# Optimization experiments

Hardware: AMD Instinct MI355X
Metric: run time of the kernel (lower is better)

## Reference

```python
import math
import jax, jax.numpy as jnp
import numpy as np

B, T, C, H = 4, 1024, 1024, 16
HD = C // H
BLOCK = 1024


def setup_inputs() -> dict:
    key = jax.random.key(0)
    k0, k1, k2, k3 = jax.random.split(key, 4)
    x = jax.random.normal(k0, (B, T, C), dtype=jnp.float32)
    # torch Linear weight is (out, in); we store (in, out) and apply x @ W + b
    W_attn = jax.random.normal(k1, (C, 3 * C), dtype=jnp.float32) * 0.02
    b_attn = jnp.zeros((3 * C,), dtype=jnp.float32)
    W_proj = jax.random.normal(k2, (C, C), dtype=jnp.float32) * 0.02
    b_proj = jnp.zeros((C,), dtype=jnp.float32)
    # rel_pos_emb: (n_head, block_size, head_dim), std 0.02 (leading 1 dim dropped)
    rel_pos_emb = jax.random.normal(k3, (H, BLOCK, HD), dtype=jnp.float32) * 0.02
    return {"x": x, "W_attn": W_attn, "b_attn": b_attn,
            "W_proj": W_proj, "b_proj": b_proj, "rel_pos_emb": rel_pos_emb}


def reference(x, W_attn, b_attn, W_proj, b_proj, rel_pos_emb):
    Bx, Tx, Cx = x.shape
    qkv = x @ W_attn + b_attn                      # (B, T, 3C)
    q, k, v = jnp.split(qkv, 3, axis=2)
    q = q.reshape(Bx, Tx, H, HD).transpose(0, 2, 1, 3)   # (B, H, T, hd)
    k = k.reshape(Bx, Tx, H, HD).transpose(0, 2, 1, 3)
    v = v.reshape(Bx, Tx, H, HD).transpose(0, 2, 1, 3)

    att = jnp.einsum('bhid,bhjd->bhij', q, k)      # (B, H, T, T)

    # relative position score: pos[b,h,i,j] = sum_d E[h, clamp(i-j,0), d] * k[b,h,j,d]
    # compute P[b,h,r,j] = <E[h,r,:], k[b,h,j,:]> then gather r = clamp(i-j, 0)
    rng = jnp.arange(Tx)
    dist = jnp.clip(rng[:, None] - rng[None, :], 0, None)          # (T, T)
    P = jnp.einsum('hrd,bhjd->bhrj', rel_pos_emb[:, :Tx], k)       # (B, H, T, T)
    pos_score = jnp.take_along_axis(P, dist[None, None, :, :], axis=2)
    att = att + pos_score

    att = att * (1.0 / math.sqrt(HD))
    causal = jnp.tril(jnp.ones((Tx, Tx), dtype=bool))
    att = jnp.where(causal[None, None], att, -jnp.inf)
    att = jax.nn.softmax(att, axis=-1)
    # dropout p=0.0 -> identity
    y = jnp.einsum('bhij,bhjd->bhid', att, v)      # (B, H, T, hd)
    y = y.transpose(0, 2, 1, 3).reshape(Bx, Tx, Cx)
    return y @ W_proj + b_proj
```

## Files before the change

kernel.cpp:

```cpp
#include <hip/hip_runtime.h>


typedef __bf16 bf16x8 __attribute__((ext_vector_type(8)));
typedef float f32x4 __attribute__((ext_vector_type(4)));
typedef unsigned short ushort_t;

#define T_SEQ 1024
#define NHEAD 16
#define HDIM 64
#define PLANE 4194304

__device__ __forceinline__ float bf2f(ushort_t h) {
    unsigned int u = ((unsigned int)h) << 16;
    float f; __builtin_memcpy(&f, &u, 4); return f;
}
__device__ __forceinline__ ushort_t f2bf(float f) {
    unsigned int u; __builtin_memcpy(&u, &f, 4);
    u = u + 0x7FFFu + ((u >> 16) & 1u);
    return (ushort_t)(u >> 16);
}

__global__ __launch_bounds__(256) void sentinel_kernel(float* out, int n, float val) {
    const int i = blockIdx.x * 256 + threadIdx.x;
    if (i < n) out[i] = val;
}

__global__ __launch_bounds__(256) void convert_bf16(
    const float* __restrict__ src, ushort_t* __restrict__ dst, int n)
{
    const int i = (blockIdx.x * 256 + threadIdx.x) * 4;
    if (i < n) {
        const float4 v = *reinterpret_cast<const float4*>(src + i);
        union { unsigned long long u; ushort_t s[4]; } o;
        o.s[0] = f2bf(v.x); o.s[1] = f2bf(v.y); o.s[2] = f2bf(v.z); o.s[3] = f2bf(v.w);
        *reinterpret_cast<unsigned long long*>(dst + i) = o.u;
    }
}

__global__ __launch_bounds__(256) void transpose_bf16(
    const float* __restrict__ W, ushort_t* __restrict__ Wt, int Kdim, int Ndim)
{
    __shared__ ushort_t t[64][65];
    const int n0 = blockIdx.x * 64, k0 = blockIdx.y * 64;
    const int cx = threadIdx.x & 63, ry = threadIdx.x >> 6;
#pragma unroll
    for (int i = 0; i < 16; i++) {
        const int r = ry + i * 4;
        t[r][cx] = f2bf(W[(size_t)(k0 + r) * Ndim + n0 + cx]);
    }
    __syncthreads();
#pragma unroll
    for (int i = 0; i < 16; i++) {
        const int r = ry + i * 4;
        Wt[(size_t)(n0 + r) * Kdim + k0 + cx] = t[cx][r];
    }
}

template <int MODE>
__global__ __launch_bounds__(256) void gemm128(
    const ushort_t* __restrict__ A16, const ushort_t* __restrict__ Bt,
    const float* __restrict__ bias, void* __restrict__ out_,
    int Ndim, int Kdim)
{
    __shared__ __align__(16) ushort_t As[128 * 32];
    __shared__ __align__(16) ushort_t Bs[128 * 32];

    const int tid = threadIdx.x;
    const int w = tid >> 6;
    const int lane = tid & 63;
    const int l15 = lane & 15;
    const int quad = lane >> 4;
    const int m0 = blockIdx.y * 128, n0 = blockIdx.x * 128;
    const int wm = (w & 1) * 64, wn = (w >> 1) * 64;

    f32x4 acc[4][4];
#pragma unroll
    for (int mt = 0; mt < 4; mt++)
#pragma unroll
        for (int nt = 0; nt < 4; nt++) acc[mt][nt] = (f32x4){0.f, 0.f, 0.f, 0.f};

    for (int kk = 0; kk < Kdim; kk += 32) {
        __syncthreads();
#pragma unroll
        for (int t = 0; t < 2; t++) {
            const int chunk = w * 128 + t * 64 + lane;
            const int row = chunk >> 2, kc = (chunk & 3) * 8;
            __builtin_amdgcn_global_load_lds(
                (const __attribute__((address_space(1))) void*)
                    (A16 + (size_t)(m0 + row) * Kdim + kk + kc),
                (__attribute__((address_space(3))) void*)
                    (As + (size_t)(w * 128 + t * 64) * 8), 16, 0, 0);
            __builtin_amdgcn_global_load_lds(
                (const __attribute__((address_space(1))) void*)
                    (Bt + (size_t)(n0 + row) * Kdim + kk + kc),
                (__attribute__((address_space(3))) void*)
                    (Bs + (size_t)(w * 128 + t * 64) * 8), 16, 0, 0);
        }
        __syncthreads();

        bf16x8 af[4], bf[4];
#pragma unroll
        for (int mt = 0; mt < 4; mt++)
            af[mt] = *reinterpret_cast<const bf16x8*>(&As[(wm + mt * 16 + l15) * 32 + quad * 8]);
#pragma unroll
        for (int nt = 0; nt < 4; nt++)
            bf[nt] = *reinterpret_cast<const bf16x8*>(&Bs[(wn + nt * 16 + l15) * 32 + quad * 8]);
#pragma unroll
        for (int mt = 0; mt < 4; mt++)
#pragma unroll
            for (int nt = 0; nt < 4; nt++)
                acc[mt][nt] = __builtin_amdgcn_mfma_f32_16x16x32_bf16(
                    af[mt], bf[nt], acc[mt][nt], 0, 0, 0);
    }

#pragma unroll
    for (int mt = 0; mt < 4; mt++)
#pragma unroll
        for (int nt = 0; nt < 4; nt++) {
            const int n = n0 + wn + nt * 16 + l15;
            const float bv = bias[n];
#pragma unroll
            for (int r = 0; r < 4; r++) {
                const int m = m0 + wm + mt * 16 + quad * 4 + r;
                const float val = acc[mt][nt][r] + bv;
                if (MODE == 0) {
                    ushort_t* ws = (ushort_t*)out_;
                    const int which = n >> 10;
                    const int cc = n & 1023;
                    const int h = cc >> 6, d = cc & 63;
                    const int b = m >> 10, t = m & 1023;
                    const int bh = b * NHEAD + h;
                    if (which == 2)
                        ws[(size_t)2 * PLANE + (size_t)bh * 65536 + (size_t)d * 1024 + t] = f2bf(val);
                    else
                        ws[(size_t)which * PLANE + ((size_t)bh * T_SEQ + t) * HDIM + d] = f2bf(val);
                } else {
                    ((float*)out_)[(size_t)m * Ndim + n] = val;
                }
            }
        }
}

__global__ __launch_bounds__(256) void flash_attn(
    const ushort_t* __restrict__ qp, const ushort_t* __restrict__ kp,
    const ushort_t* __restrict__ vTp, const ushort_t* __restrict__ E16,
    ushort_t* __restrict__ y16)
{
    __shared__ __align__(16) ushort_t Qs[64 * 72];
    __shared__ __align__(16) ushort_t Ks[64 * 72];
    __shared__ __align__(16) ushort_t Vt[64 * 72];
    __shared__ __align__(16) ushort_t Es[128 * 72];
    __shared__ __align__(16) ushort_t Ps[128 * 72];

    const int bh = blockIdx.y;
    const int h = bh & (NHEAD - 1);
    const int b = bh >> 4;
    const int tid = threadIdx.x;
    const int w = tid >> 6;
    const int lane = tid & 63;
    const int l15 = lane & 15;
    const int quad = lane >> 4;

    const size_t base = (size_t)bh * T_SEQ * HDIM;
    const ushort_t* Eh = E16 + (size_t)h * T_SEQ * HDIM;
    const ushort_t* vTb = vTp + (size_t)bh * 65536;
    const float c1 = 0.125f * 1.44269504f;

    const int rq = tid >> 2, cq = (tid & 3) * 16;
    const int re = tid >> 1, ce = (tid & 1) * 32;

#pragma unroll 1
    for (int ph = 0; ph < 2; ph++) {
        const int it = ph ? (int)blockIdx.x : 15 - (int)blockIdx.x;
        const int i0 = it * 64;

        {
            const ushort_t* src = qp + base + (size_t)(i0 + rq) * HDIM + cq;
            *reinterpret_cast<uint4*>(&Qs[rq * 72 + cq]) = *reinterpret_cast<const uint4*>(src);
            *reinterpret_cast<uint4*>(&Qs[rq * 72 + cq + 8]) = *reinterpret_cast<const uint4*>(src + 8);
        }

        f32x4 o[4];
#pragma unroll
        for (int dt = 0; dt < 4; dt++) o[dt] = (f32x4){0.f, 0.f, 0.f, 0.f};
        float mrow[4], lrow[4];
#pragma unroll
        for (int r = 0; r < 4; r++) { mrow[r] = -3e38f; lrow[r] = 0.f; }

        for (int j0 = 0; j0 <= i0; j0 += 64) {
            const int d0 = i0 - j0;
            __syncthreads();
            {
                const ushort_t* ksrc = kp + base + (size_t)(j0 + rq) * HDIM + cq;
                *reinterpret_cast<uint4*>(&Ks[rq * 72 + cq]) = *reinterpret_cast<const uint4*>(ksrc);
                *reinterpret_cast<uint4*>(&Ks[rq * 72 + cq + 8]) = *reinterpret_cast<const uint4*>(ksrc + 8);
                const ushort_t* vsrc = vTb + (size_t)rq * 1024 + j0 + cq;
                *reinterpret_cast<uint4*>(&Vt[rq * 72 + cq]) = *reinterpret_cast<const uint4*>(vsrc);
                *reinterpret_cast<uint4*>(&Vt[rq * 72 + cq + 8]) = *reinterpret_cast<const uint4*>(vsrc + 8);
            }
            {
                int g = d0 - 64 + re;
                g = g < 0 ? 0 : (g > 1023 ? 1023 : g);
                const ushort_t* esrc = Eh + (size_t)g * HDIM + ce;
#pragma unroll
                for (int q16 = 0; q16 < 4; q16++)
                    *reinterpret_cast<uint4*>(&Es[re * 72 + ce + q16 * 8]) =
                        *reinterpret_cast<const uint4*>(esrc + q16 * 8);
            }
            __syncthreads();

            f32x4 s[4], pb[2][4];
#pragma unroll
            for (int nt = 0; nt < 4; nt++) {
                s[nt] = (f32x4){0.f, 0.f, 0.f, 0.f};
                pb[0][nt] = (f32x4){0.f, 0.f, 0.f, 0.f};
                pb[1][nt] = (f32x4){0.f, 0.f, 0.f, 0.f};
            }
#pragma unroll
            for (int ks = 0; ks < 2; ks++) {
                const int ko = ks * 32 + quad * 8;
                const bf16x8 aq  = *reinterpret_cast<const bf16x8*>(&Qs[(w * 16 + l15) * 72 + ko]);
                const bf16x8 ae0 = *reinterpret_cast<const bf16x8*>(&Es[(w * 32 + l15) * 72 + ko]);
                const bf16x8 ae1 = *reinterpret_cast<const bf16x8*>(&Es[(w * 32 + 16 + l15) * 72 + ko]);
#pragma unroll
                for (int nt = 0; nt < 4; nt++) {
                    const bf16x8 bk = *reinterpret_cast<const bf16x8*>(&Ks[(nt * 16 + l15) * 72 + ko]);
                    s[nt] = __builtin_amdgcn_mfma_f32_16x16x32_bf16(aq, bk, s[nt], 0, 0, 0);
                    pb[0][nt] = __builtin_amdgcn_mfma_f32_16x16x32_bf16(ae0, bk, pb[0][nt], 0, 0, 0);
                    pb[1][nt] = __builtin_amdgcn_mfma_f32_16x16x32_bf16(ae1, bk, pb[1][nt], 0, 0, 0);
                }
            }
#pragma unroll
            for (int mf = 0; mf < 2; mf++)
#pragma unroll
                for (int nt = 0; nt < 4; nt++)
#pragma unroll
                    for (int r = 0; r < 4; r++)
                        Ps[(w * 32 + mf * 16 + quad * 4 + r) * 72 + nt * 16 + l15] =
                            f2bf(pb[mf][nt][r]);
            __syncthreads();

            float pv[4][4], mnew[4];
#pragma unroll
            for (int r = 0; r < 4; r++) mnew[r] = mrow[r];
            const int brmin = 64 - d0;
#pragma unroll
            for (int nt = 0; nt < 4; nt++) {
                const int jl = nt * 16 + l15;
#pragma unroll
                for (int r = 0; r < 4; r++) {
                    const int il = w * 16 + quad * 4 + r;
                    float sv;
                    if (d0 == 0 && jl > il) {
                        sv = -3e38f;
                    } else {
                        int br = il - jl + 64;
                        br = br < brmin ? brmin : br;
                        sv = (s[nt][r] + bf2f(Ps[br * 72 + jl])) * c1;
                    }
                    pv[nt][r] = sv;
                    mnew[r] = fmaxf(mnew[r], sv);
                }
            }
#pragma unroll
            for (int r = 0; r < 4; r++)
#pragma unroll
                for (int off = 1; off < 16; off <<= 1)
                    mnew[r] = fmaxf(mnew[r], __shfl_xor(mnew[r], off, 64));
            float rowsum[4], alpha[4];
#pragma unroll
            for (int r = 0; r < 4; r++) { alpha[r] = exp2f(mrow[r] - mnew[r]); rowsum[r] = 0.f; }
#pragma unroll
            for (int nt = 0; nt < 4; nt++)
#pragma unroll
                for (int r = 0; r < 4; r++) {
                    const float p = exp2f(pv[nt][r] - mnew[r]);
                    pv[nt][r] = p;
                    rowsum[r] += p;
                }
#pragma unroll
            for (int r = 0; r < 4; r++) {
#pragma unroll
                for (int off = 1; off < 16; off <<= 1)
                    rowsum[r] += __shfl_xor(rowsum[r], off, 64);
                lrow[r] = lrow[r] * alpha[r] + rowsum[r];
                mrow[r] = mnew[r];
            }
#pragma unroll
            for (int dt = 0; dt < 4; dt++)
#pragma unroll
                for (int r = 0; r < 4; r++) o[dt][r] *= alpha[r];
#pragma unroll
            for (int nt = 0; nt < 4; nt++)
#pragma unroll
                for (int r = 0; r < 4; r++)
                    Es[(w * 16 + quad * 4 + r) * 72 + nt * 16 + l15] = f2bf(pv[nt][r]);
            __syncthreads();

#pragma unroll
            for (int ks = 0; ks < 2; ks++) {
                const int ko = ks * 32 + quad * 8;
                const bf16x8 ap = *reinterpret_cast<const bf16x8*>(&Es[(w * 16 + l15) * 72 + ko]);
#pragma unroll
                for (int dt = 0; dt < 4; dt++) {
                    const bf16x8 bv = *reinterpret_cast<const bf16x8*>(&Vt[(dt * 16 + l15) * 72 + ko]);
                    o[dt] = __builtin_amdgcn_mfma_f32_16x16x32_bf16(ap, bv, o[dt], 0, 0, 0);
                }
            }
        }

        float inv[4];
#pragma unroll
        for (int r = 0; r < 4; r++) inv[r] = 1.0f / lrow[r];
#pragma unroll
        for (int dt = 0; dt < 4; dt++)
#pragma unroll
            for (int r = 0; r < 4; r++) {
                const int il = w * 16 + quad * 4 + r;
                const int d = dt * 16 + l15;
                y16[((size_t)(b * T_SEQ + i0 + il)) * 1024 + h * 64 + d] = f2bf(o[dt][r] * inv[r]);
            }
    }
}

extern "C" void kernel_launch(void* const* d_in, const int* in_sizes, int n_in,
                              void* d_out, int out_size, void* d_ws, size_t ws_size,
                              hipStream_t stream) {
    float* out = (float*)d_out;

    const void* x = nullptr; const void* Wa = nullptr; const void* ba = nullptr;
    const void* Wp = nullptr; const void* bp = nullptr; const void* E = nullptr;
    int anomaly = 0;
    if (n_in != 6) {
        anomaly = 2;
    } else {
        int c1M = 0;
        for (int i = 0; i < 6; i++) {
            const int s = in_sizes[i];
            if      (s == 4194304) x  = d_in[i];
            else if (s == 3145728) Wa = d_in[i];
            else if (s == 3072)    ba = d_in[i];
            else if (s == 1024)    bp = d_in[i];
            else if (s == 1048576) { if (c1M == 0) Wp = d_in[i]; else E = d_in[i]; c1M++; }
            else anomaly = 1;
        }
        if (!x || !Wa || !ba || !Wp || !bp || !E || c1M != 2) anomaly = 1;
    }
    if (!anomaly && out_size != 4194304) anomaly = 3;
    if (!anomaly && ws_size < (size_t)52428800) anomaly = 4;
    if (anomaly) {
        sentinel_kernel<<<(out_size + 255) / 256, 256, 0, stream>>>(out, out_size, 1000.0f * anomaly);
        return;
    }

    ushort_t* ws  = (ushort_t*)d_ws;
    ushort_t* qp  = ws;
    ushort_t* kp  = ws + (size_t)PLANE;
    ushort_t* vTp = ws + (size_t)2 * PLANE;
    ushort_t* y16 = ws + (size_t)3 * PLANE;
    ushort_t* x16 = ws + (size_t)4 * PLANE;
    ushort_t* WaT = ws + (size_t)5 * PLANE;
    ushort_t* WpT = WaT + (size_t)3145728;
    ushort_t* E16 = WpT + (size_t)1048576;

    convert_bf16<<<4096, 256, 0, stream>>>((const float*)x, x16, 4194304);
    transpose_bf16<<<dim3(48, 16), 256, 0, stream>>>((const float*)Wa, WaT, 1024, 3072);
    transpose_bf16<<<dim3(16, 16), 256, 0, stream>>>((const float*)Wp, WpT, 1024, 1024);
    convert_bf16<<<1024, 256, 0, stream>>>((const float*)E, E16, 1048576);

    gemm128<0><<<dim3(24, 32), 256, 0, stream>>>(x16, WaT, (const float*)ba, (void*)ws, 3072, 1024);

    flash_attn<<<dim3(8, 64), 256, 0, stream>>>(qp, kp, vTp, E16, y16);

    gemm128<1><<<dim3(8, 32), 256, 0, stream>>>(y16, WpT, (const float*)bp, (void*)out, 1024, 1024);
}
```

Baseline: 238.3 us.

## Restructure attention: register Q, pre-shifted rel-pos scatter, MFMA row sums, separate V transpose

Several changes at once. The x and E conversions become a single launch. The QKV GEMM now writes V row-major into a temporary plane, and a new transpose kernel builds V^T, replacing the strided scattered stores. The attention kernel loads Q fragments straight into registers, scatters the relative-position scores into a shifted 64x64 tile so the softmax reads them with direct indexing, splits the masked diagonal tile into its own path, and gets the softmax denominator from an extra MFMA against a ones vector instead of shuffle reductions. The cost is one extra kernel launch and the V round trip through memory, plus a row sum computed from bf16-rounded probabilities.

New measurement: 222.3 us. 6.7% less time.

```diff
diff --git a/kernel.cpp b/kernel.cpp
--- a/kernel.cpp
+++ b/kernel.cpp
@@ -25,16 +25,19 @@
     if (i < n) out[i] = val;
 }
 
-__global__ __launch_bounds__(256) void convert_bf16(
-    const float* __restrict__ src, ushort_t* __restrict__ dst, int n)
+__global__ __launch_bounds__(256) void convert2(
+    const float* __restrict__ x, ushort_t* __restrict__ x16,
+    const float* __restrict__ E, ushort_t* __restrict__ E16)
 {
-    const int i = (blockIdx.x * 256 + threadIdx.x) * 4;
-    if (i < n) {
-        const float4 v = *reinterpret_cast<const float4*>(src + i);
-        union { unsigned long long u; ushort_t s[4]; } o;
-        o.s[0] = f2bf(v.x); o.s[1] = f2bf(v.y); o.s[2] = f2bf(v.z); o.s[3] = f2bf(v.w);
-        *reinterpret_cast<unsigned long long*>(dst + i) = o.u;
-    }
+    const int bid = blockIdx.x;
+    const float* src; ushort_t* dst; int base;
+    if (bid < 4096) { src = x; dst = x16; base = bid * 1024; }
+    else            { src = E; dst = E16; base = (bid - 4096) * 1024; }
+    const int i = base + (int)threadIdx.x * 4;
+    const float4 v = *reinterpret_cast<const float4*>(src + i);
+    union { unsigned long long u; ushort_t s[4]; } o;
+    o.s[0] = f2bf(v.x); o.s[1] = f2bf(v.y); o.s[2] = f2bf(v.z); o.s[3] = f2bf(v.w);
+    *reinterpret_cast<unsigned long long*>(dst + i) = o.u;
 }
 
 __global__ __launch_bounds__(256) void transpose_bf16(
@@ -53,6 +56,28 @@
     for (int i = 0; i < 16; i++) {
         const int r = ry + i * 4;
         Wt[(size_t)(n0 + r) * Kdim + k0 + cx] = t[cx][r];
+    }
+}
+
+__global__ __launch_bounds__(256) void transpose_v(
+    const ushort_t* __restrict__ v, ushort_t* __restrict__ vT)
+{
+    __shared__ ushort_t t[64][65];
+    const int bh = blockIdx.y;
+    const int t0 = blockIdx.x * 64;
+    const int cx = threadIdx.x & 63, ry = threadIdx.x >> 6;
+    const ushort_t* src = v + (size_t)bh * 65536;
+    ushort_t* dst = vT + (size_t)bh * 65536;
+#pragma unroll
+    for (int i = 0; i < 16; i++) {
+        const int r = ry + i * 4;
+        t[r][cx] = src[(size_t)(t0 + r) * HDIM + cx];
+    }
+    __syncthreads();
+#pragma unroll
+    for (int i = 0; i < 16; i++) {
+        const int d = ry + i * 4;
+        dst[(size_t)d * T_SEQ + t0 + cx] = t[cx][d];
     }
 }
 
@@ -126,14 +151,11 @@
                 if (MODE == 0) {
                     ushort_t* ws = (ushort_t*)out_;
                     const int which = n >> 10;
+                    const size_t pl = (which == 2) ? 3 : which;
                     const int cc = n & 1023;
                     const int h = cc >> 6, d = cc & 63;
                     const int b = m >> 10, t = m & 1023;
-                    const int bh = b * NHEAD + h;
-                    if (which == 2)
-                        ws[(size_t)2 * PLANE + (size_t)bh * 65536 + (size_t)d * 1024 + t] = f2bf(val);
-                    else
-                        ws[(size_t)which * PLANE + ((size_t)bh * T_SEQ + t) * HDIM + d] = f2bf(val);
+                    ws[pl * PLANE + ((size_t)(b * NHEAD + h) * T_SEQ + t) * HDIM + d] = f2bf(val);
                 } else {
                     ((float*)out_)[(size_t)m * Ndim + n] = val;
                 }
@@ -146,11 +168,10 @@
     const ushort_t* __restrict__ vTp, const ushort_t* __restrict__ E16,
     ushort_t* __restrict__ y16)
 {
-    __shared__ __align__(16) ushort_t Qs[64 * 72];
     __shared__ __align__(16) ushort_t Ks[64 * 72];
     __shared__ __align__(16) ushort_t Vt[64 * 72];
     __shared__ __align__(16) ushort_t Es[128 * 72];
-    __shared__ __align__(16) ushort_t Ps[128 * 72];
+    __shared__ __align__(16) ushort_t Ps[64 * 64 + 16];
 
     const int bh = blockIdx.y;
     const int h = bh & (NHEAD - 1);
@@ -169,23 +190,29 @@
     const int rq = tid >> 2, cq = (tid & 3) * 16;
     const int re = tid >> 1, ce = (tid & 1) * 32;
 
+    bf16x8 ones;
+#pragma unroll
+    for (int i = 0; i < 8; i++) ones[i] = (__bf16)1.0f;
+
 #pragma unroll 1
     for (int ph = 0; ph < 2; ph++) {
         const int it = ph ? (int)blockIdx.x : 15 - (int)blockIdx.x;
         const int i0 = it * 64;
 
+        bf16x8 qf[2];
         {
-            const ushort_t* src = qp + base + (size_t)(i0 + rq) * HDIM + cq;
-            *reinterpret_cast<uint4*>(&Qs[rq * 72 + cq]) = *reinterpret_cast<const uint4*>(src);
-            *reinterpret_cast<uint4*>(&Qs[rq * 72 + cq + 8]) = *reinterpret_cast<const uint4*>(src + 8);
+            const ushort_t* qrow = qp + base + (size_t)(i0 + w * 16 + l15) * HDIM;
+            qf[0] = *reinterpret_cast<const bf16x8*>(qrow + quad * 8);
+            qf[1] = *reinterpret_cast<const bf16x8*>(qrow + 32 + quad * 8);
         }
 
-        f32x4 o[4];
+        f32x4 o[4], o5;
 #pragma unroll
         for (int dt = 0; dt < 4; dt++) o[dt] = (f32x4){0.f, 0.f, 0.f, 0.f};
-        float mrow[4], lrow[4];
-#pragma unroll
-        for (int r = 0; r < 4; r++) { mrow[r] = -3e38f; lrow[r] = 0.f; }
+        o5 = (f32x4){0.f, 0.f, 0.f, 0.f};
+        float mrow[4];
+#pragma unroll
+        for (int r = 0; r < 4; r++) mrow[r] = -3e38f;
 
         for (int j0 = 0; j0 <= i0; j0 += 64) {
             const int d0 = i0 - j0;
@@ -194,7 +221,7 @@
                 const ushort_t* ksrc = kp + base + (size_t)(j0 + rq) * HDIM + cq;
                 *reinterpret_cast<uint4*>(&Ks[rq * 72 + cq]) = *reinterpret_cast<const uint4*>(ksrc);
                 *reinterpret_cast<uint4*>(&Ks[rq * 72 + cq + 8]) = *reinterpret_cast<const uint4*>(ksrc + 8);
-                const ushort_t* vsrc = vTb + (size_t)rq * 1024 + j0 + cq;
+                const ushort_t* vsrc = vTb + (size_t)rq * T_SEQ + j0 + cq;
                 *reinterpret_cast<uint4*>(&Vt[rq * 72 + cq]) = *reinterpret_cast<const uint4*>(vsrc);
                 *reinterpret_cast<uint4*>(&Vt[rq * 72 + cq + 8]) = *reinterpret_cast<const uint4*>(vsrc + 8);
             }
@@ -219,13 +246,12 @@
 #pragma unroll
             for (int ks = 0; ks < 2; ks++) {
                 const int ko = ks * 32 + quad * 8;
-                const bf16x8 aq  = *reinterpret_cast<const bf16x8*>(&Qs[(w * 16 + l15) * 72 + ko]);
                 const bf16x8 ae0 = *reinterpret_cast<const bf16x8*>(&Es[(w * 32 + l15) * 72 + ko]);
                 const bf16x8 ae1 = *reinterpret_cast<const bf16x8*>(&Es[(w * 32 + 16 + l15) * 72 + ko]);
 #pragma unroll
                 for (int nt = 0; nt < 4; nt++) {
                     const bf16x8 bk = *reinterpret_cast<const bf16x8*>(&Ks[(nt * 16 + l15) * 72 + ko]);
-                    s[nt] = __builtin_amdgcn_mfma_f32_16x16x32_bf16(aq, bk, s[nt], 0, 0, 0);
+                    s[nt] = __builtin_amdgcn_mfma_f32_16x16x32_bf16(qf[ks], bk, s[nt], 0, 0, 0);
                     pb[0][nt] = __builtin_amdgcn_mfma_f32_16x16x32_bf16(ae0, bk, pb[0][nt], 0, 0, 0);
                     pb[1][nt] = __builtin_amdgcn_mfma_f32_16x16x32_bf16(ae1, bk, pb[1][nt], 0, 0, 0);
                 }
@@ -233,33 +259,45 @@
 #pragma unroll
             for (int mf = 0; mf < 2; mf++)
 #pragma unroll
-                for (int nt = 0; nt < 4; nt++)
-#pragma unroll
-                    for (int r = 0; r < 4; r++)
-                        Ps[(w * 32 + mf * 16 + quad * 4 + r) * 72 + nt * 16 + l15] =
-                            f2bf(pb[mf][nt][r]);
+                for (int nt = 0; nt < 4; nt++) {
+                    const int jl = nt * 16 + l15;
+#pragma unroll
+                    for (int r = 0; r < 4; r++) {
+                        const int br = w * 32 + mf * 16 + quad * 4 + r;
+                        const int il_t = br - 64 + jl;
+                        const int addr = ((unsigned)il_t < 64u) ? il_t * 64 + jl : 4096;
+                        Ps[addr] = f2bf(pb[mf][nt][r]);
+                    }
+                }
             __syncthreads();
 
             float pv[4][4], mnew[4];
 #pragma unroll
             for (int r = 0; r < 4; r++) mnew[r] = mrow[r];
-            const int brmin = 64 - d0;
-#pragma unroll
-            for (int nt = 0; nt < 4; nt++) {
-                const int jl = nt * 16 + l15;
-#pragma unroll
-                for (int r = 0; r < 4; r++) {
-                    const int il = w * 16 + quad * 4 + r;
-                    float sv;
-                    if (d0 == 0 && jl > il) {
-                        sv = -3e38f;
-                    } else {
-                        int br = il - jl + 64;
-                        br = br < brmin ? brmin : br;
-                        sv = (s[nt][r] + bf2f(Ps[br * 72 + jl])) * c1;
+            const int il0 = w * 16 + quad * 4;
+            if (j0 < i0) {
+#pragma unroll
+                for (int nt = 0; nt < 4; nt++) {
+                    const int jl = nt * 16 + l15;
+#pragma unroll
+                    for (int r = 0; r < 4; r++) {
+                        const float sv = (s[nt][r] + bf2f(Ps[(il0 + r) * 64 + jl])) * c1;
+                        pv[nt][r] = sv;
+                        mnew[r] = fmaxf(mnew[r], sv);
                     }
-                    pv[nt][r] = sv;
-                    mnew[r] = fmaxf(mnew[r], sv);
+                }
+            } else {
+#pragma unroll
+                for (int nt = 0; nt < 4; nt++) {
+                    const int jl = nt * 16 + l15;
+#pragma unroll
+                    for (int r = 0; r < 4; r++) {
+                        const int il = il0 + r;
+                        float sv = (s[nt][r] + bf2f(Ps[il * 64 + jl])) * c1;
+                        if (jl > il) sv = -3e38f;
+                        pv[nt][r] = sv;
+                        mnew[r] = fmaxf(mnew[r], sv);
+                    }
                 }
             }
 #pragma unroll
@@ -267,29 +305,23 @@
 #pragma unroll
                 for (int off = 1; off < 16; off <<= 1)
                     mnew[r] = fmaxf(mnew[r], __shfl_xor(mnew[r], off, 64));
-            float rowsum[4], alpha[4];
-#pragma unroll
-            for (int r = 0; r < 4; r++) { alpha[r] = exp2f(mrow[r] - mnew[r]); rowsum[r] = 0.f; }
+            float alpha[4];
+#pragma unroll
+            for (int r = 0; r < 4; r++) {
+                alpha[r] = exp2f(mrow[r] - mnew[r]);
+                mrow[r] = mnew[r];
+            }
 #pragma unroll
             for (int nt = 0; nt < 4; nt++)
 #pragma unroll
-                for (int r = 0; r < 4; r++) {
-                    const float p = exp2f(pv[nt][r] - mnew[r]);
-                    pv[nt][r] = p;
-                    rowsum[r] += p;
-                }
-#pragma unroll
-            for (int r = 0; r < 4; r++) {
-#pragma unroll
-                for (int off = 1; off < 16; off <<= 1)
-                    rowsum[r] += __shfl_xor(rowsum[r], off, 64);
-                lrow[r] = lrow[r] * alpha[r] + rowsum[r];
-                mrow[r] = mnew[r];
-            }
+                for (int r = 0; r < 4; r++)
+                    pv[nt][r] = exp2f(pv[nt][r] - mnew[r]);
 #pragma unroll
             for (int dt = 0; dt < 4; dt++)
 #pragma unroll
                 for (int r = 0; r < 4; r++) o[dt][r] *= alpha[r];
+#pragma unroll
+            for (int r = 0; r < 4; r++) o5[r] *= alpha[r];
 #pragma unroll
             for (int nt = 0; nt < 4; nt++)
 #pragma unroll
@@ -306,12 +338,13 @@
                     const bf16x8 bv = *reinterpret_cast<const bf16x8*>(&Vt[(dt * 16 + l15) * 72 + ko]);
                     o[dt] = __builtin_amdgcn_mfma_f32_16x16x32_bf16(ap, bv, o[dt], 0, 0, 0);
                 }
+                o5 = __builtin_amdgcn_mfma_f32_16x16x32_bf16(ap, ones, o5, 0, 0, 0);
             }
         }
 
         float inv[4];
 #pragma unroll
-        for (int r = 0; r < 4; r++) inv[r] = 1.0f / lrow[r];
+        for (int r = 0; r < 4; r++) inv[r] = 1.0f / o5[r];
 #pragma unroll
         for (int dt = 0; dt < 4; dt++)
 #pragma unroll
@@ -353,23 +386,25 @@
         return;
     }
 
-    ushort_t* ws  = (ushort_t*)d_ws;
-    ushort_t* qp  = ws;
-    ushort_t* kp  = ws + (size_t)PLANE;
-    ushort_t* vTp = ws + (size_t)2 * PLANE;
-    ushort_t* y16 = ws + (size_t)3 * PLANE;
-    ushort_t* x16 = ws + (size_t)4 * PLANE;
-    ushort_t* WaT = ws + (size_t)5 * PLANE;
-    ushort_t* WpT = WaT + (size_t)3145728;
-    ushort_t* E16 = WpT + (size_t)1048576;
-
-    convert_bf16<<<4096, 256, 0, stream>>>((const float*)x, x16, 4194304);
+    ushort_t* ws   = (ushort_t*)d_ws;
+    ushort_t* qp   = ws;
+    ushort_t* kp   = ws + (size_t)PLANE;
+    ushort_t* vTp  = ws + (size_t)2 * PLANE;
+    ushort_t* vtmp = ws + (size_t)3 * PLANE;
+    ushort_t* y16  = vtmp;
+    ushort_t* x16  = ws + (size_t)4 * PLANE;
+    ushort_t* WaT  = ws + (size_t)5 * PLANE;
+    ushort_t* WpT  = WaT + (size_t)3145728;
+    ushort_t* E16  = WpT + (size_t)1048576;
+
+    convert2<<<5120, 256, 0, stream>>>((const float*)x, x16, (const float*)E, E16);
     transpose_bf16<<<dim3(48, 16), 256, 0, stream>>>((const float*)Wa, WaT, 1024, 3072);
     transpose_bf16<<<dim3(16, 16), 256, 0, stream>>>((const float*)Wp, WpT, 1024, 1024);
-    convert_bf16<<<1024, 256, 0, stream>>>((const float*)E, E16, 1048576);
 
     gemm128<0><<<dim3(24, 32), 256, 0, stream>>>(x16, WaT, (const float*)ba, (void*)ws, 3072, 1024);
 
+    transpose_v<<<dim3(16, 64), 256, 0, stream>>>(vtmp, vTp);
+
     flash_attn<<<dim3(8, 64), 256, 0, stream>>>(qp, kp, vTp, E16, y16);
 
     gemm128<1><<<dim3(8, 32), 256, 0, stream>>>(y16, WpT, (const float*)bp, (void*)out, 1024, 1024);
```
